# Optimization experiments

Hardware: AMD Instinct MI355X
Metric: run time of the kernel (lower is better)

Reference implementation:

```python
import jax, jax.numpy as jnp
import numpy as np

B, S, DIM, NH = 2, 2048, 1024, 8
DH = DIM // NH
GATE_SOFT_CAP = 15.0
BACKEND_EPS = 5e-05
NORM_EPS = 1e-06


def setup_inputs() -> dict:
    key = jax.random.key(0)
    kq, kk, kv, kw = jax.random.split(key, 4)
    q = jax.random.normal(kq, (B, S, DIM), dtype=jnp.float32)
    k = jax.random.normal(kk, (B, S, DIM), dtype=jnp.float32)
    v = jax.random.normal(kv, (B, S, DIM), dtype=jnp.float32)
    # ifgate: Linear(3*dim, 2*num_heads). Init weight is zeros in the module;
    # use small random weights so the gate path is non-trivial.
    ifgate_w = 0.02 * jax.random.normal(kw, (2 * NH, 3 * DIM), dtype=jnp.float32)
    # bias per reset_parameters: i_bias = -10, f_bias = linspace(3, 6, NH)
    ifgate_b = jnp.concatenate([
        jnp.full((NH,), -10.0, dtype=jnp.float32),
        jnp.linspace(3.0, 6.0, NH, dtype=jnp.float32),
    ])
    # residual-weight RMSNorm gain: effective gain = 1 + outnorm_w (init zeros)
    outnorm_w = jnp.zeros((DIM,), dtype=jnp.float32)
    return {"q": q, "k": k, "v": v, "ifgate_w": ifgate_w,
            "ifgate_b": ifgate_b, "outnorm_w": outnorm_w}


def _mlstm_parallel(q, k, v, i_pre, f_pre):
    # q,k,v: (B,NH,S,DH); i_pre,f_pre: (B,NH,S). Native stabilized parallel mLSTM.
    log_fg = jax.nn.log_sigmoid(f_pre)                       # (B,NH,S)
    lf_cs = jnp.cumsum(log_fg, axis=-1)                      # (B,NH,S)
    lf = jnp.concatenate([jnp.zeros_like(lf_cs[..., :1]), lf_cs], axis=-1)  # (B,NH,S+1)
    # log_D[t, s] = sum_{j=s+1}^{t} log_fg[j] + i_pre[s]  for s <= t, else -inf
    log_d = lf[..., 1:, None] - lf[..., None, 1:] + i_pre[..., None, :]     # (B,NH,S,S)
    t_idx = jnp.arange(q.shape[2])
    mask = t_idx[:, None] >= t_idx[None, :]
    log_d = jnp.where(mask, log_d, -jnp.inf)
    m = jnp.max(log_d, axis=-1, keepdims=True)               # (B,NH,S,1)
    d_mat = jnp.exp(log_d - m)                               # stabilized decays
    scores = jnp.einsum("bhtd,bhsd->bhts", q, k) * (1.0 / np.sqrt(DH))
    s_mat = scores * d_mat                                   # (B,NH,S,S)
    denom = jnp.maximum(jnp.abs(jnp.sum(s_mat, axis=-1, keepdims=True)),
                        jnp.exp(-m)) + BACKEND_EPS
    return jnp.einsum("bhts,bhsd->bhtd", s_mat, v) / denom   # (B,NH,S,DH)


def reference(q, k, v, ifgate_w, ifgate_b, outnorm_w):
    b, s, dim = q.shape
    # gate preactivations from concatenated q,k,v with tanh soft cap
    gate_in = jnp.concatenate([q, k, v], axis=-1)            # (B,S,3*DIM)
    pre = gate_in @ ifgate_w.T + ifgate_b                    # (B,S,2*NH)
    pre = GATE_SOFT_CAP * jnp.tanh(pre / GATE_SOFT_CAP)
    i_pre = pre[..., :NH].transpose(0, 2, 1)                 # (B,NH,S)
    f_pre = pre[..., NH:].transpose(0, 2, 1)                 # (B,NH,S)
    # split heads
    qh = q.reshape(b, s, NH, DH).transpose(0, 2, 1, 3)
    kh = k.reshape(b, s, NH, DH).transpose(0, 2, 1, 3)
    vh = v.reshape(b, s, NH, DH).transpose(0, 2, 1, 3)
    h = _mlstm_parallel(qh, kh, vh, i_pre, f_pre)            # (B,NH,S,DH)
    # multi-head RMSNorm with residual gain (bias is unused in the module's forward)
    rrms = jax.lax.rsqrt(jnp.mean(h * h, axis=-1, keepdims=True) + NORM_EPS)
    gain = (1.0 + outnorm_w).reshape(1, NH, 1, DH)
    h = h * rrms * gain
    return h.transpose(0, 2, 1, 3).reshape(b, s, dim)
```

## Files before the change

kernel.cpp:

```cpp
#include <hip/hip_runtime.h>
#include <math.h>

#define BB 2
#define SS 2048
#define DIMM 1024
#define NHH 8
#define DHH 128

constexpr float GATE_CAP = 15.0f;
constexpr float B_EPS = 5e-5f;
constexpr float N_EPS = 1e-6f;
constexpr float LOG2E = 1.4426950408889634f;
constexpr float LN_KIS = -2.4260151319598084f;

typedef _Float16 f16x8 __attribute__((ext_vector_type(8)));
typedef __fp16  h16x2 __attribute__((ext_vector_type(2)));
typedef float f32x4 __attribute__((ext_vector_type(4)));

union U8 { f16x8 v; h16x2 h[4]; unsigned int u[4]; };

__device__ inline unsigned short f2bf(float x) {
    unsigned u = __builtin_bit_cast(unsigned, x);
    unsigned r = (u + 0x7fff + ((u >> 16) & 1)) >> 16;
    return (unsigned short)r;
}
__device__ inline float bf2f(unsigned short s) {
    unsigned u = ((unsigned)s) << 16;
    return __builtin_bit_cast(float, u);
}

#define GLD_LDS16(gsrc, ldst)                                                   \
    __builtin_amdgcn_global_load_lds(                                           \
        (const __attribute__((address_space(1))) unsigned int*)(gsrc),          \
        (__attribute__((address_space(3))) unsigned int*)(ldst), 16, 0, 0)

__global__ __launch_bounds__(256) void gate_kernel(
    const float* __restrict__ q, const float* __restrict__ k, const float* __restrict__ v,
    const float* __restrict__ gw, const float* __restrict__ gb,
    float* __restrict__ i_pre, float* __restrict__ lfcs)
{
    __shared__ __align__(16) float xs[2][8][1024];

    const int tid = threadIdx.x;
    const int lane = tid & 63;
    const int wv = tid >> 6;
    const int bs0 = blockIdx.x * 8;

    const float* srcs[3] = {q, k, v};

    auto stage = [&](int buf, int i) {
        const char* src = (const char*)(srcs[i] + (size_t)bs0 * DIMM);
        #pragma unroll
        for (int j = 0; j < 8; ++j) {
            GLD_LDS16(src + j * 4096 + wv * 1024 + lane * 16,
                      (char*)&xs[buf][j][0] + wv * 1024 + lane * 16);
        }
    };

    float acc[8][4];
    #pragma unroll
    for (int r = 0; r < 8; ++r)
        #pragma unroll
        for (int o = 0; o < 4; ++o) acc[r][o] = 0.f;

    stage(0, 0);

    for (int i = 0; i < 3; ++i) {
        const int cur = i & 1;
        const float* gwi = gw + (wv * 4) * 3 * DIMM + i * DIMM;
        float4 w4[4][4];
        #pragma unroll
        for (int step = 0; step < 4; ++step)
            #pragma unroll
            for (int o = 0; o < 4; ++o)
                w4[step][o] = *(const float4*)&gwi[o * 3 * DIMM + step * 256 + lane * 4];

        if (i < 2) {
            stage(cur ^ 1, i + 1);
            asm volatile("s_waitcnt vmcnt(8)" ::: "memory");
        } else {
            asm volatile("s_waitcnt vmcnt(0)" ::: "memory");
        }
        __builtin_amdgcn_s_barrier();
        __builtin_amdgcn_sched_barrier(0);

        #pragma unroll
        for (int step = 0; step < 4; ++step) {
            #pragma unroll
            for (int r = 0; r < 8; ++r) {
                const float4 xv = *(const float4*)&xs[cur][r][step * 256 + lane * 4];
                #pragma unroll
                for (int o = 0; o < 4; ++o)
                    acc[r][o] += xv.x * w4[step][o].x + xv.y * w4[step][o].y
                               + xv.z * w4[step][o].z + xv.w * w4[step][o].w;
            }
        }
        __builtin_amdgcn_s_barrier();
    }

    #pragma unroll
    for (int r = 0; r < 8; ++r)
        #pragma unroll
        for (int o = 0; o < 4; ++o) {
            acc[r][o] += __shfl_xor(acc[r][o], 16);
            acc[r][o] += __shfl_xor(acc[r][o], 32);
        }

    float* scr = &xs[0][0][0];
    const int l16 = lane & 15;
    if (l16 == lane) {
        #pragma unroll
        for (int r = 0; r < 8; ++r) {
            float4 st = {acc[r][0], acc[r][1], acc[r][2], acc[r][3]};
            *(float4*)&scr[wv * 576 + l16 * 36 + r * 4] = st;
        }
    }
    __syncthreads();

    if (tid < 128) {
        const int row = tid & 7, o = tid >> 3;
        const float* base = &scr[(o >> 2) * 576 + row * 4 + (o & 3)];
        float s = 0.f;
        #pragma unroll
        for (int j = 0; j < 16; ++j) s += base[j * 36];
        float p = s + gb[o];
        p = GATE_CAP * tanhf(p / GATE_CAP);
        const int bs = bs0 + row;
        const int b = bs >> 11, s2 = bs & 2047;
        if (o < NHH) {
            i_pre[((size_t)b * NHH + o) * SS + s2] = p;
        } else {
            const int h = o - NHH;
            const float ls = (p >= 0.f) ? -log1pf(expf(-p)) : p - log1pf(expf(p));
            lfcs[((size_t)b * NHH + h) * SS + s2] = ls;
        }
    }
}

__global__ __launch_bounds__(256) void prep_scan(
    const float* __restrict__ k, const float* __restrict__ v,
    unsigned short* __restrict__ k16, unsigned short* __restrict__ v16,
    const float* __restrict__ i_pre,
    float* __restrict__ lfcs, float* __restrict__ mstab, float* __restrict__ aa)
{
    const int id = blockIdx.x;
    const int tid = threadIdx.x;
    __shared__ float wt[4], wm[4];

    if (id < 512) {
        const int bh = id & 15;
        const int st = id >> 4;
        const int b = bh >> 3, h = bh & 7;

        {
            const float* kp = k + ((size_t)b * SS + st * 64) * DIMM + h * DHH;
            char* kb_ = (char*)k16 + ((size_t)bh * SS + st * 64) * 256;
            #pragma unroll
            for (int j = 0; j < 8; ++j) {
                const int item = j * 256 + tid;
                const int s = item >> 5, dq = item & 31;
                float4 kx = *(const float4*)&kp[(size_t)s * DIMM + dq * 4];
                h16x2 p0 = __builtin_amdgcn_cvt_pkrtz(kx.x, kx.y);
                h16x2 p1 = __builtin_amdgcn_cvt_pkrtz(kx.z, kx.w);
                uint2 wd;
                wd.x = __builtin_bit_cast(unsigned int, p0);
                wd.y = __builtin_bit_cast(unsigned int, p1);
                *(uint2*)(kb_ + s * 256 + ((dq * 8) ^ ((s & 7) << 4))) = wd;
            }
        }
        {
            const int d2 = (tid & 63) * 2;
            const int kb = (tid >> 6) & 1;
            const int gq = tid >> 7;
            const float* vp = v + ((size_t)b * SS + st * 64 + kb * 32) * DIMM + h * DHH + d2;
            char* base = (char*)v16 + ((size_t)bh * 32 + st) * 16384;
            #pragma unroll
            for (int gg = 0; gg < 2; ++gg) {
                const int g = gq * 2 + gg;
                float2 e[8];
                #pragma unroll
                for (int j = 0; j < 8; ++j) {
                    const int s = 16 * (j >> 2) + 4 * g + (j & 3);
                    e[j] = *(const float2*)&vp[(size_t)s * DIMM];
                }
                U8 u0, u1;
                u0.h[0] = __builtin_amdgcn_cvt_pkrtz(e[0].x, e[1].x);
                u0.h[1] = __builtin_amdgcn_cvt_pkrtz(e[2].x, e[3].x);
                u0.h[2] = __builtin_amdgcn_cvt_pkrtz(e[4].x, e[5].x);
                u0.h[3] = __builtin_amdgcn_cvt_pkrtz(e[6].x, e[7].x);
                u1.h[0] = __builtin_amdgcn_cvt_pkrtz(e[0].y, e[1].y);
                u1.h[1] = __builtin_amdgcn_cvt_pkrtz(e[2].y, e[3].y);
                u1.h[2] = __builtin_amdgcn_cvt_pkrtz(e[4].y, e[5].y);
                u1.h[3] = __builtin_amdgcn_cvt_pkrtz(e[6].y, e[7].y);
                const int p0 = kb * 64 + g * 16;
                *(f16x8*)(base + d2 * 128       + (p0 ^ ((d2 & 7) << 4)))       = u0.v;
                *(f16x8*)(base + (d2 + 1) * 128 + (p0 ^ (((d2 + 1) & 7) << 4))) = u1.v;
            }
        }
        return;
    }

    const int bh = id - 512;
    const int lane = tid & 63, wv = tid >> 6;
    const size_t base = (size_t)bh * SS + tid * 8;

    float x[8];
    {
        float4 a0 = *(const float4*)&lfcs[base];
        float4 a1 = *(const float4*)&lfcs[base + 4];
        x[0] = a0.x; x[1] = a0.y; x[2] = a0.z; x[3] = a0.w;
        x[4] = a1.x; x[5] = a1.y; x[6] = a1.z; x[7] = a1.w;
    }
    #pragma unroll
    for (int i = 1; i < 8; ++i) x[i] += x[i - 1];

    const float tot = x[7];
    float inc = tot;
    #pragma unroll
    for (int off = 1; off < 64; off <<= 1) {
        float n = __shfl_up(inc, off);
        if (lane >= off) inc += n;
    }
    const float exc = inc - tot;

    if (lane == 63) wt[wv] = inc;
    __syncthreads();
    float wpre = 0.f;
    for (int w = 0; w < 4; ++w) if (w < wv) wpre += wt[w];
    const float off0 = exc + wpre;
    #pragma unroll
    for (int i = 0; i < 8; ++i) x[i] += off0;
    {
        float4 s0 = {x[0], x[1], x[2], x[3]}, s1 = {x[4], x[5], x[6], x[7]};
        *(float4*)&lfcs[base] = s0;
        *(float4*)&lfcs[base + 4] = s1;
    }

    float g[8];
    {
        float4 i0 = *(const float4*)&i_pre[base];
        float4 i1 = *(const float4*)&i_pre[base + 4];
        g[0] = i0.x - x[0]; g[1] = i0.y - x[1]; g[2] = i0.z - x[2]; g[3] = i0.w - x[3];
        g[4] = i1.x - x[4]; g[5] = i1.y - x[5]; g[6] = i1.z - x[6]; g[7] = i1.w - x[7];
        float4 s0 = {g[0] * LOG2E, g[1] * LOG2E, g[2] * LOG2E, g[3] * LOG2E};
        float4 s1 = {g[4] * LOG2E, g[5] * LOG2E, g[6] * LOG2E, g[7] * LOG2E};
        *(float4*)&aa[base] = s0;
        *(float4*)&aa[base + 4] = s1;
    }
    float mg[8];
    mg[0] = g[0];
    #pragma unroll
    for (int i = 1; i < 8; ++i) mg[i] = fmaxf(mg[i - 1], g[i]);

    float minc = mg[7];
    #pragma unroll
    for (int off = 1; off < 64; off <<= 1) {
        float n = __shfl_up(minc, off);
        if (lane >= off) minc = fmaxf(minc, n);
    }
    float mexc = __shfl_up(minc, 1);
    if (lane == 0) mexc = -1e30f;
    if (lane == 63) wm[wv] = minc;
    __syncthreads();
    float wmpre = -1e30f;
    for (int w = 0; w < 4; ++w) if (w < wv) wmpre = fmaxf(wmpre, wm[w]);
    const float pm = fmaxf(mexc, wmpre);
    float4 s0, s1;
    s0.x = x[0] + fmaxf(pm, mg[0]); s0.y = x[1] + fmaxf(pm, mg[1]);
    s0.z = x[2] + fmaxf(pm, mg[2]); s0.w = x[3] + fmaxf(pm, mg[3]);
    s1.x = x[4] + fmaxf(pm, mg[4]); s1.y = x[5] + fmaxf(pm, mg[5]);
    s1.z = x[6] + fmaxf(pm, mg[6]); s1.w = x[7] + fmaxf(pm, mg[7]);
    *(float4*)&mstab[base] = s0;
    *(float4*)&mstab[base + 4] = s1;
}

__global__ __launch_bounds__(256, 2) void mlstm_splitk(
    const float* __restrict__ q,
    const unsigned short* __restrict__ k16, const unsigned short* __restrict__ v16,
    const float* __restrict__ lfcs, const float* __restrict__ aa,
    unsigned short* __restrict__ pnum, float* __restrict__ pden)
{
    __shared__ __align__(16) unsigned short kbuf[2][8192];
    __shared__ __align__(16) unsigned short vbuf[2][8192];

    const int tid = threadIdx.x;
    const int lane = tid & 63;
    const int wv = tid >> 6;
    const int g = lane >> 4;
    const int l16 = lane & 15;

    const int id = blockIdx.x;
    int bh, qq, chunk;
    if (id < 256) {
        bh = id & 15;
        const int j = id >> 4;
        if (j < 7)       { qq = 5 + j;               chunk = 0; }
        else if (j == 7) { qq = 11;                  chunk = 1; }
        else             { qq = 12 + ((j - 8) >> 1); chunk = (j - 8) & 1; }
    } else {
        const int e = id - 256;
        bh = e & 15;
        const int j = e >> 4;
        if (j < 5)       { qq = j;             chunk = 0; }
        else if (j < 10) { qq = 6 + (j - 5);   chunk = 1; }
        else             { qq = 12 + (j - 10); chunk = 2; }
    }
    const int b = bh >> 3, h = bh & 7;
    const int tw0 = qq * 128 + 32 * wv;

    const size_t bhS = (size_t)bh * SS;
    const float* qp = q + (size_t)b * SS * DIMM + h * DHH;
    const char* kg = (const char*)k16 + (size_t)bh * 524288;
    const char* vg = (const char*)v16 + (size_t)bh * 524288;

    f16x8 qf[2][4];
    float cdec2[2];
    #pragma unroll
    for (int nt = 0; nt < 2; ++nt) {
        const int t = tw0 + 16 * nt + l16;
        cdec2[nt] = (lfcs[bhS + t] + LN_KIS) * LOG2E;
        const float* qrow = qp + (size_t)t * DIMM;
        #pragma unroll
        for (int kb = 0; kb < 4; ++kb) {
            float4 x0 = *(const float4*)&qrow[kb * 32 + g * 8];
            float4 x1 = *(const float4*)&qrow[kb * 32 + g * 8 + 4];
            U8 uu;
            uu.h[0] = __builtin_amdgcn_cvt_pkrtz(x0.x, x0.y);
            uu.h[1] = __builtin_amdgcn_cvt_pkrtz(x0.z, x0.w);
            uu.h[2] = __builtin_amdgcn_cvt_pkrtz(x1.x, x1.y);
            uu.h[3] = __builtin_amdgcn_cvt_pkrtz(x1.z, x1.w);
            qf[nt][kb] = uu.v;
        }
    }

    f32x4 oacc[2][8];
    #pragma unroll
    for (int nt = 0; nt < 2; ++nt)
        #pragma unroll
        for (int mt = 0; mt < 8; ++mt)
            oacc[nt][mt] = (f32x4){0.f, 0.f, 0.f, 0.f};
    float dpart[2] = {0.f, 0.f};

    const int st0 = chunk * 12;
    const int st1m = 2 * qq + 1;
    const int st1 = (st0 + 11 < st1m) ? (st0 + 11) : st1m;

    auto stage = [&](int bi, int st) {
        const char* ksrc = kg + (size_t)st * 16384;
        const char* vsrc = vg + (size_t)st * 16384;
        #pragma unroll
        for (int j = 0; j < 4; ++j) {
            const int off = (j * 4 + wv) * 1024;
            GLD_LDS16(ksrc + off + lane * 16, (char*)&kbuf[bi][0] + off);
            GLD_LDS16(vsrc + off + lane * 16, (char*)&vbuf[bi][0] + off);
        }
    };

    stage(0, st0);

    for (int st = st0; st <= st1; ++st) {
        const int cur = (st - st0) & 1;
        const float* ap = aa + bhS + st * 64;
        f32x4 av[4];
        av[0] = *(const f32x4*)&ap[g * 4];
        av[1] = *(const f32x4*)&ap[16 + g * 4];
        av[2] = *(const f32x4*)&ap[32 + g * 4];
        av[3] = *(const f32x4*)&ap[48 + g * 4];

        if (st < st1) {
            stage(cur ^ 1, st + 1);
            asm volatile("s_waitcnt vmcnt(8)" ::: "memory");
        } else {
            asm volatile("s_waitcnt vmcnt(0)" ::: "memory");
        }
        __builtin_amdgcn_s_barrier();
        __builtin_amdgcn_sched_barrier(0);

        const int s0 = st * 64;
        const bool diag = (st >= 2 * qq);

        f32x4 stacc[2][4];
        #pragma unroll
        for (int nt = 0; nt < 2; ++nt)
            #pragma unroll
            for (int ct = 0; ct < 4; ++ct)
                stacc[nt][ct] = (f32x4){0.f, 0.f, 0.f, 0.f};

        f16x8 pf[2][2];

        #define QKT_PAIR(CT0)                                                            \
            __builtin_amdgcn_s_setprio(1);                                               \
            _Pragma("unroll")                                                            \
            for (int ct = CT0; ct < CT0 + 2; ++ct) {                                     \
                const int row = ct * 16 + l16;                                           \
                _Pragma("unroll")                                                        \
                for (int kb = 0; kb < 4; ++kb) {                                         \
                    f16x8 kf = *(const f16x8*)((const char*)&kbuf[cur][0] +              \
                                ((row * 256 + kb * 64 + g * 16) ^ ((row & 7) << 4)));    \
                    stacc[0][ct] = __builtin_amdgcn_mfma_f32_16x16x32_f16(kf, qf[0][kb], stacc[0][ct], 0, 0, 0); \
                    stacc[1][ct] = __builtin_amdgcn_mfma_f32_16x16x32_f16(kf, qf[1][kb], stacc[1][ct], 0, 0, 0); \
                }                                                                        \
            }                                                                            \
            __builtin_amdgcn_s_setprio(0);

        #define DECAY_PACK(KB)                                                           \
            _Pragma("unroll")                                                            \
            for (int nt = 0; nt < 2; ++nt) {                                             \
                float dsum = 0.f;                                                        \
                const int t_idx = tw0 + nt * 16 + l16;                                   \
                _Pragma("unroll")                                                        \
                for (int ct = 2 * (KB); ct < 2 * (KB) + 2; ++ct) {                       \
                    _Pragma("unroll")                                                    \
                    for (int i = 0; i < 4; ++i) {                                        \
                        const float e = __builtin_amdgcn_exp2f(cdec2[nt] + av[ct][i]);   \
                        float val = stacc[nt][ct][i] * e;                                \
                        if (diag && (s0 + ct * 16 + g * 4 + i > t_idx)) val = 0.f;       \
                        dsum += val;                                                     \
                        stacc[nt][ct][i] = val;                                          \
                    }                                                                    \
                }                                                                        \
                dpart[nt] += dsum;                                                       \
                U8 uu;                                                                   \
                uu.h[0] = __builtin_amdgcn_cvt_pkrtz(stacc[nt][2*(KB)][0],   stacc[nt][2*(KB)][1]);   \
                uu.h[1] = __builtin_amdgcn_cvt_pkrtz(stacc[nt][2*(KB)][2],   stacc[nt][2*(KB)][3]);   \
                uu.h[2] = __builtin_amdgcn_cvt_pkrtz(stacc[nt][2*(KB)+1][0], stacc[nt][2*(KB)+1][1]); \
                uu.h[3] = __builtin_amdgcn_cvt_pkrtz(stacc[nt][2*(KB)+1][2], stacc[nt][2*(KB)+1][3]); \
                pf[nt][KB] = uu.v;                                                       \
            }

        #define PV_HALF(KB)                                                              \
            __builtin_amdgcn_s_setprio(1);                                               \
            _Pragma("unroll")                                                            \
            for (int mt = 0; mt < 8; ++mt) {                                             \
                const int dI = mt * 16 + l16;                                            \
                f16x8 vf = *(const f16x8*)((const char*)&vbuf[cur][0] +                  \
                            dI * 128 + (((KB) * 64 + g * 16) ^ ((dI & 7) << 4)));        \
                oacc[0][mt] = __builtin_amdgcn_mfma_f32_16x16x32_f16(vf, pf[0][KB], oacc[0][mt], 0, 0, 0); \
                oacc[1][mt] = __builtin_amdgcn_mfma_f32_16x16x32_f16(vf, pf[1][KB], oacc[1][mt], 0, 0, 0); \
            }                                                                            \
            __builtin_amdgcn_s_setprio(0);

        QKT_PAIR(0)
        DECAY_PACK(0)
        QKT_PAIR(2)
        PV_HALF(0)
        DECAY_PACK(1)
        PV_HALF(1)

        #undef QKT_PAIR
        #undef DECAY_PACK
        #undef PV_HALF

        __builtin_amdgcn_sched_barrier(0);
        __builtin_amdgcn_s_barrier();
    }

    const int uoff = (qq < 6) ? qq : ((qq < 12) ? (6 + 2 * (qq - 6)) : (18 + 3 * (qq - 12)));
    const size_t cidx = (size_t)bh * 30 + uoff + chunk;
    #pragma unroll
    for (int nt = 0; nt < 2; ++nt) {
        float den = dpart[nt];
        den += __shfl_xor(den, 16);
        den += __shfl_xor(den, 32);
        const int row = wv * 32 + nt * 16 + l16;
        if (g == 0) pden[cidx * 128 + row] = den;
        #pragma unroll
        for (int mt = 0; mt < 8; ++mt) {
            ushort4 pk;
            pk.x = f2bf(oacc[nt][mt][0]);
            pk.y = f2bf(oacc[nt][mt][1]);
            pk.z = f2bf(oacc[nt][mt][2]);
            pk.w = f2bf(oacc[nt][mt][3]);
            *(ushort4*)&pnum[((cidx * 64 + wv * 16 + nt * 8 + mt) << 8) + lane * 4] = pk;
        }
    }
}

__global__ __launch_bounds__(256) void reduce_kernel(
    const unsigned short* __restrict__ pnum, const float* __restrict__ pden,
    const float* __restrict__ mstab, const float* __restrict__ onw,
    float* __restrict__ out)
{
    const int id = blockIdx.x;
    const int bh = id & 15;
    const int qq = id >> 4;
    const int b = bh >> 3, h = bh & 7;
    const int tid = threadIdx.x;
    const int lane = tid & 63;
    const int wv = tid >> 6;
    const int g = lane >> 4;
    const int l16 = lane & 15;

    const int nch = (qq < 6) ? 1 : ((qq < 12) ? 2 : 3);
    const int uoff = (qq < 6) ? qq : ((qq < 12) ? (6 + 2 * (qq - 6)) : (18 + 3 * (qq - 12)));
    const size_t cbase = (size_t)bh * 30 + uoff;

    f32x4 acc[2][8];
    #pragma unroll
    for (int nt = 0; nt < 2; ++nt)
        #pragma unroll
        for (int mt = 0; mt < 8; ++mt)
            acc[nt][mt] = (f32x4){0.f, 0.f, 0.f, 0.f};
    float den[2] = {0.f, 0.f};

    for (int c = 0; c < nch; ++c) {
        const size_t fb = (cbase + c) * 64 + wv * 16;
        #pragma unroll
        for (int nt = 0; nt < 2; ++nt) {
            #pragma unroll
            for (int mt = 0; mt < 8; ++mt) {
                ushort4 t4 = *(const ushort4*)&pnum[((fb + nt * 8 + mt) << 8) + lane * 4];
                acc[nt][mt][0] += bf2f(t4.x);
                acc[nt][mt][1] += bf2f(t4.y);
                acc[nt][mt][2] += bf2f(t4.z);
                acc[nt][mt][3] += bf2f(t4.w);
            }
            den[nt] += pden[(cbase + c) * 128 + wv * 32 + nt * 16 + l16];
        }
    }

    #pragma unroll
    for (int nt = 0; nt < 2; ++nt) {
        const int t = qq * 128 + wv * 32 + nt * 16 + l16;
        const float m = mstab[(size_t)bh * SS + t];
        const float em = __expf(-m);
        const float dt = den[nt] * em;
        const float denf = fmaxf(fabsf(dt), em) + B_EPS;
        const float inv = em / denf;
        float ssq = 0.f;
        #pragma unroll
        for (int mt = 0; mt < 8; ++mt) {
            #pragma unroll
            for (int i = 0; i < 4; ++i) {
                acc[nt][mt][i] *= inv;
                ssq += acc[nt][mt][i] * acc[nt][mt][i];
            }
        }
        ssq += __shfl_xor(ssq, 16);
        ssq += __shfl_xor(ssq, 32);
        const float rms = rsqrtf(ssq * (1.0f / DHH) + N_EPS);

        float* orow = out + ((size_t)b * SS + t) * DIMM + h * DHH;
        #pragma unroll
        for (int mt = 0; mt < 8; ++mt) {
            float4 gn = *(const float4*)&onw[h * DHH + mt * 16 + g * 4];
            float4 o4;
            o4.x = acc[nt][mt][0] * rms * (1.f + gn.x);
            o4.y = acc[nt][mt][1] * rms * (1.f + gn.y);
            o4.z = acc[nt][mt][2] * rms * (1.f + gn.z);
            o4.w = acc[nt][mt][3] * rms * (1.f + gn.w);
            *(float4*)&orow[mt * 16 + g * 4] = o4;
        }
    }
}

extern "C" void kernel_launch(void* const* d_in, const int* in_sizes, int n_in,
                              void* d_out, int out_size, void* d_ws, size_t ws_size,
                              hipStream_t stream) {
    const float* q   = (const float*)d_in[0];
    const float* k   = (const float*)d_in[1];
    const float* v   = (const float*)d_in[2];
    const float* gw  = (const float*)d_in[3];
    const float* gb  = (const float*)d_in[4];
    const float* onw = (const float*)d_in[5];
    float* out = (float*)d_out;

    float* ws    = (float*)d_ws;
    float* i_pre = ws;
    float* lfcs  = ws + 32768;
    float* mm    = ws + 65536;
    float* aa    = ws + 98304;
    float* pden  = ws + 131072;
    unsigned short* pnum = (unsigned short*)((char*)d_ws + 1048576);
    unsigned short* k16  = (unsigned short*)((char*)d_ws + 16777216);
    unsigned short* v16  = (unsigned short*)((char*)d_ws + 25165824);

    hipLaunchKernelGGL(gate_kernel, dim3(BB * SS / 8), dim3(256), 0, stream,
                       q, k, v, gw, gb, i_pre, lfcs);
    hipLaunchKernelGGL(prep_scan, dim3(528), dim3(256), 0, stream,
                       k, v, k16, v16, i_pre, lfcs, mm, aa);
    hipLaunchKernelGGL(mlstm_splitk, dim3(480), dim3(256), 0, stream,
                       q, k16, v16, lfcs, aa, pnum, pden);
    hipLaunchKernelGGL(reduce_kernel, dim3(16 * 16), dim3(256), 0, stream,
                       pnum, pden, mm, onw, out);
}
```

Measured before the change: 80.35 us.

## Fuse K fp16 conversion into gate kernel and refine split-K chunking to 6 tiles

The gate kernel already stages k rows in LDS, so it now also converts them to swizzled fp16 and writes k16 directly. The prep kernel therefore no longer rereads k from global memory. Separately, the split-K attention kernel now uses chunks of 6 key tiles instead of 12, with a lookup table mapping 51 slots per head to (query block, chunk). This raises the grid from 480 to 816 blocks to even out per-block work. The costs are more partial-result traffic and larger reduce work for late query blocks (up to 6 chunks), and the workspace offsets for k16/v16 are moved.

```diff
diff --git a/kernel.cpp b/kernel.cpp
--- a/kernel.cpp
+++ b/kernel.cpp
@@ -6,6 +6,7 @@
 #define DIMM 1024
 #define NHH 8
 #define DHH 128
+#define NSLOT 51
 
 constexpr float GATE_CAP = 15.0f;
 constexpr float B_EPS = 5e-5f;
@@ -19,6 +20,17 @@
 
 union U8 { f16x8 v; h16x2 h[4]; unsigned int u[4]; };
 
+__device__ __constant__ unsigned char SLOT2QQ[NSLOT] = {
+    15,15,15,15,15,15, 14,14,14,14,14, 13,13,13,13,13, 12,12,12,12,12,
+    11,11,11,11, 10,10,10,10, 9,9,9,9, 8,8,8, 7,7,7, 6,6,6,
+    5,5, 4,4, 3,3, 2, 1, 0};
+__device__ __constant__ unsigned char SLOT2CH[NSLOT] = {
+    0,1,2,3,4,5, 0,1,2,3,4, 0,1,2,3,4, 0,1,2,3,4,
+    0,1,2,3, 0,1,2,3, 0,1,2,3, 0,1,2, 0,1,2, 0,1,2,
+    0,1, 0,1, 0,1, 0, 0, 0};
+__device__ __constant__ unsigned char QQ2BASE[16] = {50,49,48,46,44,42,39,36,33,29,25,21,16,11,6,0};
+__device__ __constant__ unsigned char QQ2NCH[16]  = {1,1,1,2,2,2,3,3,3,4,4,4,5,5,5,6};
+
 __device__ inline unsigned short f2bf(float x) {
     unsigned u = __builtin_bit_cast(unsigned, x);
     unsigned r = (u + 0x7fff + ((u >> 16) & 1)) >> 16;
@@ -37,7 +49,8 @@
 __global__ __launch_bounds__(256) void gate_kernel(
     const float* __restrict__ q, const float* __restrict__ k, const float* __restrict__ v,
     const float* __restrict__ gw, const float* __restrict__ gb,
-    float* __restrict__ i_pre, float* __restrict__ lfcs)
+    float* __restrict__ i_pre, float* __restrict__ lfcs,
+    unsigned short* __restrict__ k16)
 {
     __shared__ __align__(16) float xs[2][8][1024];
 
@@ -96,6 +109,25 @@
             }
         }
         __builtin_amdgcn_s_barrier();
+    }
+
+    #pragma unroll
+    for (int it = 0; it < 8; ++it) {
+        const int item = it * 256 + tid;
+        const int r = item >> 8;
+        const int dq = item & 255;
+        const int hh = dq >> 5;
+        const int dd4 = dq & 31;
+        float4 kx = *(const float4*)&xs[1][r][dq * 4];
+        h16x2 p0 = __builtin_amdgcn_cvt_pkrtz(kx.x, kx.y);
+        h16x2 p1 = __builtin_amdgcn_cvt_pkrtz(kx.z, kx.w);
+        uint2 wd;
+        wd.x = __builtin_bit_cast(unsigned int, p0);
+        wd.y = __builtin_bit_cast(unsigned int, p1);
+        const int bs = bs0 + r;
+        const int b = bs >> 11, s2 = bs & 2047;
+        const size_t bh = (size_t)b * NHH + hh;
+        *(uint2*)((char*)k16 + (bh * 2048 + s2) * 256 + ((dd4 * 8) ^ ((s2 & 7) << 4))) = wd;
     }
 
     #pragma unroll
@@ -137,9 +169,8 @@
     }
 }
 
-__global__ __launch_bounds__(256) void prep_scan(
-    const float* __restrict__ k, const float* __restrict__ v,
-    unsigned short* __restrict__ k16, unsigned short* __restrict__ v16,
+__global__ __launch_bounds__(256) void vscan_kernel(
+    const float* __restrict__ v, unsigned short* __restrict__ v16,
     const float* __restrict__ i_pre,
     float* __restrict__ lfcs, float* __restrict__ mstab, float* __restrict__ aa)
 {
@@ -151,51 +182,32 @@
         const int bh = id & 15;
         const int st = id >> 4;
         const int b = bh >> 3, h = bh & 7;
-
-        {
-            const float* kp = k + ((size_t)b * SS + st * 64) * DIMM + h * DHH;
-            char* kb_ = (char*)k16 + ((size_t)bh * SS + st * 64) * 256;
+        const int d2 = (tid & 63) * 2;
+        const int kb = (tid >> 6) & 1;
+        const int gq = tid >> 7;
+        const float* vp = v + ((size_t)b * SS + st * 64 + kb * 32) * DIMM + h * DHH + d2;
+        char* base = (char*)v16 + ((size_t)bh * 32 + st) * 16384;
+        #pragma unroll
+        for (int gg = 0; gg < 2; ++gg) {
+            const int g = gq * 2 + gg;
+            float2 e[8];
             #pragma unroll
             for (int j = 0; j < 8; ++j) {
-                const int item = j * 256 + tid;
-                const int s = item >> 5, dq = item & 31;
-                float4 kx = *(const float4*)&kp[(size_t)s * DIMM + dq * 4];
-                h16x2 p0 = __builtin_amdgcn_cvt_pkrtz(kx.x, kx.y);
-                h16x2 p1 = __builtin_amdgcn_cvt_pkrtz(kx.z, kx.w);
-                uint2 wd;
-                wd.x = __builtin_bit_cast(unsigned int, p0);
-                wd.y = __builtin_bit_cast(unsigned int, p1);
-                *(uint2*)(kb_ + s * 256 + ((dq * 8) ^ ((s & 7) << 4))) = wd;
+                const int s = 16 * (j >> 2) + 4 * g + (j & 3);
+                e[j] = *(const float2*)&vp[(size_t)s * DIMM];
             }
-        }
-        {
-            const int d2 = (tid & 63) * 2;
-            const int kb = (tid >> 6) & 1;
-            const int gq = tid >> 7;
-            const float* vp = v + ((size_t)b * SS + st * 64 + kb * 32) * DIMM + h * DHH + d2;
-            char* base = (char*)v16 + ((size_t)bh * 32 + st) * 16384;
-            #pragma unroll
-            for (int gg = 0; gg < 2; ++gg) {
-                const int g = gq * 2 + gg;
-                float2 e[8];
-                #pragma unroll
-                for (int j = 0; j < 8; ++j) {
-                    const int s = 16 * (j >> 2) + 4 * g + (j & 3);
-                    e[j] = *(const float2*)&vp[(size_t)s * DIMM];
-                }
-                U8 u0, u1;
-                u0.h[0] = __builtin_amdgcn_cvt_pkrtz(e[0].x, e[1].x);
-                u0.h[1] = __builtin_amdgcn_cvt_pkrtz(e[2].x, e[3].x);
-                u0.h[2] = __builtin_amdgcn_cvt_pkrtz(e[4].x, e[5].x);
-                u0.h[3] = __builtin_amdgcn_cvt_pkrtz(e[6].x, e[7].x);
-                u1.h[0] = __builtin_amdgcn_cvt_pkrtz(e[0].y, e[1].y);
-                u1.h[1] = __builtin_amdgcn_cvt_pkrtz(e[2].y, e[3].y);
-                u1.h[2] = __builtin_amdgcn_cvt_pkrtz(e[4].y, e[5].y);
-                u1.h[3] = __builtin_amdgcn_cvt_pkrtz(e[6].y, e[7].y);
-                const int p0 = kb * 64 + g * 16;
-                *(f16x8*)(base + d2 * 128       + (p0 ^ ((d2 & 7) << 4)))       = u0.v;
-                *(f16x8*)(base + (d2 + 1) * 128 + (p0 ^ (((d2 + 1) & 7) << 4))) = u1.v;
-            }
+            U8 u0, u1;
+            u0.h[0] = __builtin_amdgcn_cvt_pkrtz(e[0].x, e[1].x);
+            u0.h[1] = __builtin_amdgcn_cvt_pkrtz(e[2].x, e[3].x);
+            u0.h[2] = __builtin_amdgcn_cvt_pkrtz(e[4].x, e[5].x);
+            u0.h[3] = __builtin_amdgcn_cvt_pkrtz(e[6].x, e[7].x);
+            u1.h[0] = __builtin_amdgcn_cvt_pkrtz(e[0].y, e[1].y);
+            u1.h[1] = __builtin_amdgcn_cvt_pkrtz(e[2].y, e[3].y);
+            u1.h[2] = __builtin_amdgcn_cvt_pkrtz(e[4].y, e[5].y);
+            u1.h[3] = __builtin_amdgcn_cvt_pkrtz(e[6].y, e[7].y);
+            const int p0 = kb * 64 + g * 16;
+            *(f16x8*)(base + d2 * 128       + (p0 ^ ((d2 & 7) << 4)))       = u0.v;
+            *(f16x8*)(base + (d2 + 1) * 128 + (p0 ^ (((d2 + 1) & 7) << 4))) = u1.v;
         }
         return;
     }
@@ -290,21 +302,10 @@
     const int l16 = lane & 15;
 
     const int id = blockIdx.x;
-    int bh, qq, chunk;
-    if (id < 256) {
-        bh = id & 15;
-        const int j = id >> 4;
-        if (j < 7)       { qq = 5 + j;               chunk = 0; }
-        else if (j == 7) { qq = 11;                  chunk = 1; }
-        else             { qq = 12 + ((j - 8) >> 1); chunk = (j - 8) & 1; }
-    } else {
-        const int e = id - 256;
-        bh = e & 15;
-        const int j = e >> 4;
-        if (j < 5)       { qq = j;             chunk = 0; }
-        else if (j < 10) { qq = 6 + (j - 5);   chunk = 1; }
-        else             { qq = 12 + (j - 10); chunk = 2; }
-    }
+    const int bh = id & 15;
+    const int slot = id >> 4;
+    const int qq = SLOT2QQ[slot];
+    const int chunk = SLOT2CH[slot];
     const int b = bh >> 3, h = bh & 7;
     const int tw0 = qq * 128 + 32 * wv;
 
@@ -341,9 +342,9 @@
             oacc[nt][mt] = (f32x4){0.f, 0.f, 0.f, 0.f};
     float dpart[2] = {0.f, 0.f};
 
-    const int st0 = chunk * 12;
+    const int st0 = chunk * 6;
     const int st1m = 2 * qq + 1;
-    const int st1 = (st0 + 11 < st1m) ? (st0 + 11) : st1m;
+    const int st1 = (st0 + 5 < st1m) ? (st0 + 5) : st1m;
 
     auto stage = [&](int bi, int st) {
         const char* ksrc = kg + (size_t)st * 16384;
@@ -455,8 +456,7 @@
         __builtin_amdgcn_s_barrier();
     }
 
-    const int uoff = (qq < 6) ? qq : ((qq < 12) ? (6 + 2 * (qq - 6)) : (18 + 3 * (qq - 12)));
-    const size_t cidx = (size_t)bh * 30 + uoff + chunk;
+    const size_t cidx = (size_t)bh * NSLOT + slot;
     #pragma unroll
     for (int nt = 0; nt < 2; ++nt) {
         float den = dpart[nt];
@@ -491,9 +491,8 @@
     const int g = lane >> 4;
     const int l16 = lane & 15;
 
-    const int nch = (qq < 6) ? 1 : ((qq < 12) ? 2 : 3);
-    const int uoff = (qq < 6) ? qq : ((qq < 12) ? (6 + 2 * (qq - 6)) : (18 + 3 * (qq - 12)));
-    const size_t cbase = (size_t)bh * 30 + uoff;
+    const int nch = QQ2NCH[qq];
+    const size_t cbase = (size_t)bh * NSLOT + QQ2BASE[qq];
 
     f32x4 acc[2][8];
     #pragma unroll
@@ -572,14 +571,14 @@
     float* aa    = ws + 98304;
     float* pden  = ws + 131072;
     unsigned short* pnum = (unsigned short*)((char*)d_ws + 1048576);
-    unsigned short* k16  = (unsigned short*)((char*)d_ws + 16777216);
-    unsigned short* v16  = (unsigned short*)((char*)d_ws + 25165824);
+    unsigned short* k16  = (unsigned short*)((char*)d_ws + 29360128);
+    unsigned short* v16  = (unsigned short*)((char*)d_ws + 37748736);
 
     hipLaunchKernelGGL(gate_kernel, dim3(BB * SS / 8), dim3(256), 0, stream,
-                       q, k, v, gw, gb, i_pre, lfcs);
-    hipLaunchKernelGGL(prep_scan, dim3(528), dim3(256), 0, stream,
-                       k, v, k16, v16, i_pre, lfcs, mm, aa);
-    hipLaunchKernelGGL(mlstm_splitk, dim3(480), dim3(256), 0, stream,
+                       q, k, v, gw, gb, i_pre, lfcs, k16);
+    hipLaunchKernelGGL(vscan_kernel, dim3(528), dim3(256), 0, stream,
+                       v, v16, i_pre, lfcs, mm, aa);
+    hipLaunchKernelGGL(mlstm_splitk, dim3(16 * NSLOT), dim3(256), 0, stream,
                        q, k16, v16, lfcs, aa, pnum, pden);
     hipLaunchKernelGGL(reduce_kernel, dim3(16 * 16), dim3(256), 0, stream,
                        pnum, pden, mm, onw, out);
```

New measurement: 76.50 us. 4.8% less time.
